# Kernel tuning notes

Measured on AMD Instinct MI355X. Metric: run time of the kernel, lower is better.

Reference implementation:

```python
import jax, jax.numpy as jnp
import numpy as np
from jax import lax

B, S, LQ, LS, D, F, FS, K, V = 32, 32, 30, 40, 300, 256, 3, 5, 100000


def setup_inputs() -> dict:
    key = jax.random.key(0)
    ks = jax.random.split(key, 8)
    return {
        "question": jax.random.randint(ks[0], (B, LQ), 0, V),
        "sentences": jax.random.randint(ks[1], (B, S, LS), 0, V),
        "target_sents": jax.random.randint(ks[2], (B, S), 0, 2),
        "target_docs": jax.random.randint(ks[3], (B,), 0, 2),
        "similarity_one_hot": (jax.random.uniform(ks[4], (B, S, LQ, LS)) < 0.05).astype(jnp.float32),
        "embeds": jax.random.normal(ks[5], (V, D), jnp.float32) * 0.1,
        "filters": jax.random.normal(ks[6], (F, FS, D), jnp.float32) * 0.1,
        "lin_w": jax.random.normal(ks[7], (6,), jnp.float32) * 0.3,
        "lin_b": jnp.zeros((), jnp.float32),
    }


def _conv_seq(x, W):
    # x: [..., L, D]; W: [F, fs, D]. Mirrors F.conv2d with padding=(fs//2+1, 0)
    # followed by keeping the LAST L output rows.
    fs = W.shape[1]
    pad = fs // 2 + 1
    L = x.shape[-2]
    lead = x.shape[:-2]
    xf = x.reshape((-1, L, x.shape[-1])).transpose(0, 2, 1)          # [N, D, L]
    out = lax.conv_general_dilated(
        xf, W.transpose(0, 2, 1), (1,), [(pad, pad)],
        dimension_numbers=("NCH", "OIH", "NCH"))                      # [N, F, L+2]
    out = out[:, :, -L:].transpose(0, 2, 1)                           # [N, L, F]
    return out.reshape(lead + (L, W.shape[0]))


def _cosine(Q, Sx):
    # Q: [B, LQ, d]; Sx: [B, S, LS, d] -> [B, S, LQ, LS]
    num = jnp.einsum("bqd,bsld->bsql", Q, Sx)
    qn = jnp.sqrt(jnp.sum(Q * Q, axis=-1))        # [B, LQ]
    sn = jnp.sqrt(jnp.sum(Sx * Sx, axis=-1))      # [B, S, LS]
    return num / (qn[:, None, :, None] * sn[:, :, None, :])


def _pool(sim):
    # sort + take top-k over last axis == top_k; features = (max, mean-of-top-k)
    vals = lax.top_k(sim, K)[0]                   # [..., K], descending
    return jnp.stack([vals[..., 0], vals.mean(-1)], axis=-1)  # [..., 2]


def _bce(p, t):
    logp = jnp.clip(jnp.log(p), -100.0)
    log1p = jnp.clip(jnp.log(1.0 - p), -100.0)
    return -(t * logp + (1.0 - t) * log1p).mean()


def reference(question, sentences, target_sents, target_docs, similarity_one_hot,
              embeds, filters, lin_w, lin_b):
    qe = embeds[question]                          # [B, LQ, D]
    se = embeds[sentences]                         # [B, S, LS, D]
    qc = _conv_seq(qe, filters)                    # [B, LQ, F]
    sc = _conv_seq(se, filters)                    # [B, S, LS, F]

    sim_ins = _cosine(qe, se)                      # [B, S, LQ, LS]
    sim_sen = _cosine(qc, sc)                      # [B, S, LQ, LS]

    feats = jnp.concatenate(
        [_pool(sim_ins), _pool(sim_sen), _pool(similarity_one_hot)], axis=-1)  # [B,S,LQ,6]
    lo = jax.nn.sigmoid(jnp.einsum("bsqf,f->bsq", feats, lin_w) + lin_b)        # [B,S,LQ]
    sent_output = lo.mean(-1)                      # [B, S]

    sent_loss = _bce_per_doc_mean(sent_output, target_sents.astype(jnp.float32))
    doc_em = sent_output.max(-1)                   # [B]
    doc_loss = _bce(doc_em, target_docs.astype(jnp.float32))
    total_loss = (sent_loss + doc_loss) / 2.0
    return (total_loss, sent_output, doc_em)


def _bce_per_doc_mean(p, t):
    # mean over docs of per-doc BCE (each a mean over sentences); equals global mean
    logp = jnp.clip(jnp.log(p), -100.0)
    log1p = jnp.clip(jnp.log(1.0 - p), -100.0)
    return -(t * logp + (1.0 - t) * log1p).mean(-1).mean()
```

## Files before the change

kernel.cpp:

```cpp
#include <hip/hip_runtime.h>
#include <math.h>


typedef __attribute__((ext_vector_type(4))) float f32x4;
typedef __attribute__((ext_vector_type(8))) short s16x8;

__device__ inline ushort bf16rne(float f) {
  unsigned u = __float_as_uint(f);
  u += 0x7fff + ((u >> 16) & 1);
  return (ushort)(u >> 16);
}
__device__ inline uint pack2(float a, float b) {
  return (uint)bf16rne(a) | ((uint)bf16rne(b) << 16);
}
__device__ inline float ubf(short h) { return __uint_as_float(((uint)(ushort)h) << 16); }

__global__ __launch_bounds__(64) void k_prepB(const float* __restrict__ filters,
                                              ushort* __restrict__ fB) {
  const int bid = blockIdx.x;
  const int lane = threadIdx.x;
  const int nt = bid & 15;
  const int tk = bid >> 4;
  const int tap = tk / 10, kstep = tk - tap * 10;
  const int f = nt * 16 + (lane & 15);
  const int kb = kstep * 32 + (lane >> 4) * 8;
  uint p[4];
#pragma unroll
  for (int h = 0; h < 4; ++h) {
    int d0 = kb + h * 2, d1 = kb + h * 2 + 1;
    float v0 = (d0 < 300) ? filters[(size_t)f * 900 + tap * 300 + d0] : 0.f;
    float v1 = (d1 < 300) ? filters[(size_t)f * 900 + tap * 300 + d1] : 0.f;
    p[h] = (uint)bf16rne(v0) | ((uint)bf16rne(v1) << 16);
  }
  uint4* dst = (uint4*)(fB + ((size_t)bid * 64 + lane) * 8);
  *dst = make_uint4(p[0], p[1], p[2], p[3]);
}

template<int L, int MT, int ROWS_ST>
__global__ __launch_bounds__(256) void k_conv_mfma(const int* __restrict__ tokens,
                                                   const float* __restrict__ embeds,
                                                   const ushort* __restrict__ fB,
                                                   ushort* __restrict__ blobA,
                                                   ushort* __restrict__ blobC,
                                                   float* __restrict__ rcpA,
                                                   float* __restrict__ rcpC) {
  constexpr int R320 = ROWS_ST * 320;
  __shared__ __align__(16) ushort xs[R320];
  __shared__ int tok[64];
  const int tid = threadIdx.x;
  const int seq = blockIdx.x;

  if (tid < L) tok[tid] = tokens[(size_t)seq * L + tid];
  __syncthreads();

  for (int idx = tid; idx < ROWS_ST * 80; idx += 256) {
    int row = idx / 80;
    int s = idx - row * 80;
    int d = s * 4;
    float4 v = make_float4(0.f, 0.f, 0.f, 0.f);
    if (row < L && d < 300) v = *(const float4*)(embeds + (size_t)tok[row] * 300 + d);
    int flat = row * 320 + d;
    int swz = flat ^ ((row & 7) << 3);
    *(uint2*)(xs + swz) = make_uint2(pack2(v.x, v.y), pack2(v.z, v.w));
  }
  __syncthreads();

  const int wv = tid >> 6, lane = tid & 63;
  const int lr = lane & 15, lh = lane >> 4;

  for (int t = wv; t < 10 * MT; t += 4) {
    int kstep = t / MT, tile = t - kstep * MT;
    int row = tile * 16 + lr;
    int flat = row * 320 + kstep * 32 + lh * 8;
    s16x8 v = *(const s16x8*)(xs + (flat ^ ((row & 7) << 3)));
    *(s16x8*)(blobA + ((((size_t)seq * 10 + kstep) * MT + tile) * 64 + lane) * 8) = v;
  }
  if (tid < L) {
    int row = tid;
    float s = 0.f;
    for (int c = 0; c < 40; ++c) {
      int flat = row * 320 + c * 8;
      s16x8 v = *(const s16x8*)(xs + (flat ^ ((row & 7) << 3)));
#pragma unroll
      for (int i = 0; i < 8; ++i) { float f = ubf(v[i]); s += f * f; }
    }
    rcpA[(size_t)seq * L + row] = (s > 0.f) ? rsqrtf(s) : 0.f;
  }

  f32x4 acc[MT][4];
#pragma unroll
  for (int mt = 0; mt < MT; ++mt)
#pragma unroll
    for (int n = 0; n < 4; ++n)
#pragma unroll
      for (int r = 0; r < 4; ++r) acc[mt][n][r] = 0.f;

  const s16x8* fBv = (const s16x8*)fB;
  for (int kstep = 0; kstep < 10; ++kstep) {
#pragma unroll
    for (int tap = 0; tap < 3; ++tap) {
      s16x8 b[4];
#pragma unroll
      for (int n = 0; n < 4; ++n)
        b[n] = fBv[((size_t)((tap * 10 + kstep) * 16 + (wv * 4 + n))) * 64 + lane];
#pragma unroll
      for (int mt = 0; mt < MT; ++mt) {
        int row = mt * 16 + lr + tap;
        int flat = row * 320 + kstep * 32 + lh * 8;
        s16x8 a = *(const s16x8*)(xs + (flat ^ ((row & 7) << 3)));
#pragma unroll
        for (int n = 0; n < 4; ++n)
          acc[mt][n] = __builtin_amdgcn_mfma_f32_16x16x32_bf16(a, b[n], acc[mt][n], 0, 0, 0);
      }
    }
  }
  __syncthreads();

#pragma unroll
  for (int mt = 0; mt < MT; ++mt)
#pragma unroll
    for (int n = 0; n < 4; ++n)
#pragma unroll
      for (int r = 0; r < 4; ++r) {
        int j = mt * 16 + lh * 4 + r;
        if (j < L) {
          int f = wv * 64 + n * 16 + lr;
          int flat = j * 320 + f;
          xs[flat ^ ((j & 7) << 3)] = bf16rne(acc[mt][n][r]);
        }
      }
  __syncthreads();

  for (int t = wv; t < 8 * MT; t += 4) {
    int kstep = t / MT, tile = t - kstep * MT;
    int row = tile * 16 + lr;
    int flat = row * 320 + kstep * 32 + lh * 8;
    s16x8 v = *(const s16x8*)(xs + (flat ^ ((row & 7) << 3)));
    *(s16x8*)(blobC + ((((size_t)seq * 8 + kstep) * MT + tile) * 64 + lane) * 8) = v;
  }
  if (tid < L) {
    int row = tid;
    float s = 0.f;
    for (int c = 0; c < 32; ++c) {
      int flat = row * 320 + c * 8;
      s16x8 v = *(const s16x8*)(xs + (flat ^ ((row & 7) << 3)));
#pragma unroll
      for (int i = 0; i < 8; ++i) { float f = ubf(v[i]); s += f * f; }
    }
    rcpC[(size_t)seq * L + row] = (s > 0.f) ? rsqrtf(s) : 0.f;
  }
}

__global__ __launch_bounds__(256, 6) void k_sim(const float* __restrict__ oneh,
                                                const ushort* __restrict__ qeb,
                                                const ushort* __restrict__ seb,
                                                const ushort* __restrict__ qcb,
                                                const ushort* __restrict__ scb,
                                                const float* __restrict__ rq0,
                                                const float* __restrict__ rs0,
                                                const float* __restrict__ rq1,
                                                const float* __restrict__ rs1,
                                                const float* __restrict__ lin_w,
                                                const float* __restrict__ lin_b,
                                                float* __restrict__ out) {
  const int bs = blockIdx.x;
  const int b = bs >> 5;
  const int tid = threadIdx.x;
  const int wv = tid >> 6, lane = tid & 63;
  const int lr = lane & 15, lh = lane >> 4;

  __shared__ float simb[2][30][49];
  __shared__ float ohl[30 * 41];
  __shared__ float rQ[2][30], rS[2][40];
  __shared__ float feats[30][6];
  __shared__ float lo[30];

  if (tid < 30) rQ[0][tid] = rq0[b * 30 + tid];
  else if (tid < 60) rQ[1][tid - 30] = rq1[b * 30 + (tid - 30)];
  else if (tid < 100) rS[0][tid - 60] = rs0[(size_t)bs * 40 + (tid - 60)];
  else if (tid < 140) rS[1][tid - 100] = rs1[(size_t)bs * 40 + (tid - 100)];
  {
    const float* og = oneh + (size_t)bs * 1200;
    for (int i = tid; i < 1200; i += 256) {
      int q = i / 40, l = i - q * 40;
      ohl[q * 41 + l] = og[i];
    }
  }
  __syncthreads();

  for (int task = wv; task < 6; task += 4) {
    int ph = task / 3, nt = task - ph * 3;
    int KS = ph ? 8 : 10;
    const ushort* Ab = ph ? (qcb + (size_t)b * 8 * 2 * 512) : (qeb + (size_t)b * 10 * 2 * 512);
    const ushort* Bb = ph ? (scb + (size_t)bs * 8 * 3 * 512) : (seb + (size_t)bs * 10 * 3 * 512);
    f32x4 acc0 = {0.f, 0.f, 0.f, 0.f};
    f32x4 acc1 = {0.f, 0.f, 0.f, 0.f};
    for (int k = 0; k < KS; ++k) {
      s16x8 bf = *(const s16x8*)(Bb + ((size_t)(k * 3 + nt) * 64 + lane) * 8);
      s16x8 a0 = *(const s16x8*)(Ab + ((size_t)(k * 2 + 0) * 64 + lane) * 8);
      s16x8 a1 = *(const s16x8*)(Ab + ((size_t)(k * 2 + 1) * 64 + lane) * 8);
      acc0 = __builtin_amdgcn_mfma_f32_16x16x32_bf16(a0, bf, acc0, 0, 0, 0);
      acc1 = __builtin_amdgcn_mfma_f32_16x16x32_bf16(a1, bf, acc1, 0, 0, 0);
    }
    int l = nt * 16 + lr;
    if (l < 40) {
#pragma unroll
      for (int r = 0; r < 4; ++r) {
        int q0 = lh * 4 + r;
        simb[ph][q0][l] = acc0[r] * rQ[ph][q0] * rS[ph][l];
        int q1 = 16 + lh * 4 + r;
        if (q1 < 30) simb[ph][q1][l] = acc1[r] * rQ[ph][q1] * rS[ph][l];
      }
    }
  }
  __syncthreads();

  if (tid < 90) {
    const int m = tid / 30, q = tid - m * 30;
    const float* row = (m == 0) ? &simb[0][q][0] : (m == 1) ? &simb[1][q][0] : (ohl + q * 41);
    float thr = 3.4e38f;
    int got = 0;
    float sum = 0.f, maxv = 0.f;
    while (got < 5) {
      float mx = -3.4e38f;
      int c = 0;
      for (int l = 0; l < 40; ++l) {
        float v = row[l];
        if (v < thr) {
          if (v > mx) { mx = v; c = 1; }
          else if (v == mx) { c++; }
        }
      }
      if (c == 0) break;
      if (got == 0) maxv = mx;
      int take = (c < 5 - got) ? c : (5 - got);
      sum += mx * (float)take;
      got += take;
      thr = mx;
    }
    feats[q][m * 2 + 0] = maxv;
    feats[q][m * 2 + 1] = sum * 0.2f;
  }
  __syncthreads();
  if (tid < 30) {
    float z = lin_b[0];
#pragma unroll
    for (int i = 0; i < 6; ++i) z += feats[tid][i] * lin_w[i];
    lo[tid] = 1.0f / (1.0f + expf(-z));
  }
  __syncthreads();
  if (tid == 0) {
    float sum = 0.f;
    for (int q = 0; q < 30; ++q) sum += lo[q];
    out[1 + bs] = sum * (1.0f / 30.0f);
  }
}

__global__ __launch_bounds__(256) void k_loss(const int* __restrict__ tsent,
                                              const int* __restrict__ tdoc,
                                              float* __restrict__ out) {
  __shared__ float red[256];
  __shared__ float sent_loss_sh;
  const int tid = threadIdx.x;
  float local = 0.f;
  for (int i = tid; i < 1024; i += 256) {
    float p = out[1 + i];
    float t = (float)tsent[i];
    float lp = fmaxf(logf(p), -100.f);
    float l1 = fmaxf(logf(1.f - p), -100.f);
    local += -(t * lp + (1.f - t) * l1);
  }
  red[tid] = local;
  __syncthreads();
  for (int off = 128; off > 0; off >>= 1) {
    if (tid < off) red[tid] += red[tid + off];
    __syncthreads();
  }
  if (tid == 0) sent_loss_sh = red[0] * (1.0f / 1024.0f);
  __syncthreads();
  float dterm = 0.f;
  if (tid < 32) {
    float mx = out[1 + tid * 32];
    for (int s2 = 1; s2 < 32; ++s2) mx = fmaxf(mx, out[1 + tid * 32 + s2]);
    out[1025 + tid] = mx;
    float t = (float)tdoc[tid];
    float lp = fmaxf(logf(mx), -100.f);
    float l1 = fmaxf(logf(1.f - mx), -100.f);
    dterm = -(t * lp + (1.f - t) * l1);
  }
  red[tid] = dterm;
  __syncthreads();
  for (int off = 128; off > 0; off >>= 1) {
    if (tid < off) red[tid] += red[tid + off];
    __syncthreads();
  }
  if (tid == 0) out[0] = 0.5f * (sent_loss_sh + red[0] * (1.0f / 32.0f));
}

extern "C" void kernel_launch(void* const* d_in, const int* in_sizes, int n_in,
                              void* d_out, int out_size, void* d_ws, size_t ws_size,
                              hipStream_t stream) {
  const int*   question     = (const int*)d_in[0];
  const int*   sentences    = (const int*)d_in[1];
  const int*   target_sents = (const int*)d_in[2];
  const int*   target_docs  = (const int*)d_in[3];
  const float* oneh         = (const float*)d_in[4];
  const float* embeds       = (const float*)d_in[5];
  const float* filters      = (const float*)d_in[6];
  const float* lin_w        = (const float*)d_in[7];
  const float* lin_b        = (const float*)d_in[8];
  float* out = (float*)d_out;

  ushort* fB  = (ushort*)d_ws;
  ushort* seb = fB  + 245760;
  ushort* scb = seb + 15728640;
  ushort* qeb = scb + 12582912;
  ushort* qcb = qeb + 327680;
  float*  rs0 = (float*)(qcb + 262144);
  float*  rs1 = rs0 + 40960;
  float*  rq0 = rs1 + 40960;
  float*  rq1 = rq0 + 960;

  k_prepB<<<480, 64, 0, stream>>>(filters, fB);
  k_conv_mfma<40, 3, 50><<<1024, 256, 0, stream>>>(sentences, embeds, fB, seb, scb, rs0, rs1);
  k_conv_mfma<30, 2, 34><<<32, 256, 0, stream>>>(question, embeds, fB, qeb, qcb, rq0, rq1);
  k_sim<<<1024, 256, 0, stream>>>(oneh, qeb, seb, qcb, scb, rq0, rs0, rq1, rs1,
                                  lin_w, lin_b, out);
  k_loss<<<1, 256, 0, stream>>>(target_sents, target_docs, out);
}
```

Before: 98.62 us.

## Fuse sentence conv into similarity kernel to avoid global intermediates

```diff
diff --git a/kernel.cpp b/kernel.cpp
--- a/kernel.cpp
+++ b/kernel.cpp
@@ -151,34 +151,36 @@
   }
 }
 
-__global__ __launch_bounds__(256, 6) void k_sim(const float* __restrict__ oneh,
-                                                const ushort* __restrict__ qeb,
-                                                const ushort* __restrict__ seb,
-                                                const ushort* __restrict__ qcb,
-                                                const ushort* __restrict__ scb,
-                                                const float* __restrict__ rq0,
-                                                const float* __restrict__ rs0,
-                                                const float* __restrict__ rq1,
-                                                const float* __restrict__ rs1,
-                                                const float* __restrict__ lin_w,
-                                                const float* __restrict__ lin_b,
-                                                float* __restrict__ out) {
+__global__ __launch_bounds__(256) void k_fused(const int* __restrict__ sentences,
+                                               const float* __restrict__ embeds,
+                                               const ushort* __restrict__ fB,
+                                               const ushort* __restrict__ qeb,
+                                               const ushort* __restrict__ qcb,
+                                               const float* __restrict__ rq0,
+                                               const float* __restrict__ rq1,
+                                               const float* __restrict__ oneh,
+                                               const float* __restrict__ lin_w,
+                                               const float* __restrict__ lin_b,
+                                               float* __restrict__ out) {
+  constexpr int L = 40, MT = 3, ROWS_ST = 50;
+  constexpr int R320 = ROWS_ST * 320;
+  __shared__ __align__(16) ushort xs[R320];
+  __shared__ int tok[48];
+  __shared__ float simb[2][30][49];
+  __shared__ float ohl[30 * 41];
+  __shared__ float rQ[2][30], rS[2][40];
+  __shared__ float feats[30][6];
+  __shared__ float lo[30];
+
   const int bs = blockIdx.x;
   const int b = bs >> 5;
   const int tid = threadIdx.x;
   const int wv = tid >> 6, lane = tid & 63;
   const int lr = lane & 15, lh = lane >> 4;
 
-  __shared__ float simb[2][30][49];
-  __shared__ float ohl[30 * 41];
-  __shared__ float rQ[2][30], rS[2][40];
-  __shared__ float feats[30][6];
-  __shared__ float lo[30];
-
-  if (tid < 30) rQ[0][tid] = rq0[b * 30 + tid];
-  else if (tid < 60) rQ[1][tid - 30] = rq1[b * 30 + (tid - 30)];
-  else if (tid < 100) rS[0][tid - 60] = rs0[(size_t)bs * 40 + (tid - 60)];
-  else if (tid < 140) rS[1][tid - 100] = rs1[(size_t)bs * 40 + (tid - 100)];
+  if (tid < 40) tok[tid] = sentences[(size_t)bs * 40 + tid];
+  else if (tid >= 64 && tid < 94) rQ[0][tid - 64] = rq0[b * 30 + (tid - 64)];
+  else if (tid >= 96 && tid < 126) rQ[1][tid - 96] = rq1[b * 30 + (tid - 96)];
   {
     const float* og = oneh + (size_t)bs * 1200;
     for (int i = tid; i < 1200; i += 256) {
@@ -188,28 +190,130 @@
   }
   __syncthreads();
 
-  for (int task = wv; task < 6; task += 4) {
-    int ph = task / 3, nt = task - ph * 3;
-    int KS = ph ? 8 : 10;
-    const ushort* Ab = ph ? (qcb + (size_t)b * 8 * 2 * 512) : (qeb + (size_t)b * 10 * 2 * 512);
-    const ushort* Bb = ph ? (scb + (size_t)bs * 8 * 3 * 512) : (seb + (size_t)bs * 10 * 3 * 512);
-    f32x4 acc0 = {0.f, 0.f, 0.f, 0.f};
-    f32x4 acc1 = {0.f, 0.f, 0.f, 0.f};
-    for (int k = 0; k < KS; ++k) {
-      s16x8 bf = *(const s16x8*)(Bb + ((size_t)(k * 3 + nt) * 64 + lane) * 8);
+  for (int idx = tid; idx < ROWS_ST * 80; idx += 256) {
+    int row = idx / 80;
+    int s = idx - row * 80;
+    int d = s * 4;
+    float4 v = make_float4(0.f, 0.f, 0.f, 0.f);
+    if (row < L && d < 300) v = *(const float4*)(embeds + (size_t)tok[row] * 300 + d);
+    int flat = row * 320 + d;
+    int swz = flat ^ ((row & 7) << 3);
+    *(uint2*)(xs + swz) = make_uint2(pack2(v.x, v.y), pack2(v.z, v.w));
+  }
+  __syncthreads();
+
+  f32x4 s0a = {0.f, 0.f, 0.f, 0.f}, s0b = {0.f, 0.f, 0.f, 0.f};
+  if (wv < 3) {
+    const ushort* Ab = qeb + (size_t)b * 10 * 2 * 512;
+    for (int k = 0; k < 10; ++k) {
+      int brow = wv * 16 + lr;
+      int bflat = brow * 320 + k * 32 + lh * 8;
+      s16x8 bf = *(const s16x8*)(xs + (bflat ^ ((brow & 7) << 3)));
       s16x8 a0 = *(const s16x8*)(Ab + ((size_t)(k * 2 + 0) * 64 + lane) * 8);
       s16x8 a1 = *(const s16x8*)(Ab + ((size_t)(k * 2 + 1) * 64 + lane) * 8);
-      acc0 = __builtin_amdgcn_mfma_f32_16x16x32_bf16(a0, bf, acc0, 0, 0, 0);
-      acc1 = __builtin_amdgcn_mfma_f32_16x16x32_bf16(a1, bf, acc1, 0, 0, 0);
-    }
-    int l = nt * 16 + lr;
+      s0a = __builtin_amdgcn_mfma_f32_16x16x32_bf16(a0, bf, s0a, 0, 0, 0);
+      s0b = __builtin_amdgcn_mfma_f32_16x16x32_bf16(a1, bf, s0b, 0, 0, 0);
+    }
+  } else if (lane < 40) {
+    float s = 0.f;
+    for (int c = 0; c < 40; ++c) {
+      int flat = lane * 320 + c * 8;
+      s16x8 v = *(const s16x8*)(xs + (flat ^ ((lane & 7) << 3)));
+#pragma unroll
+      for (int i = 0; i < 8; ++i) { float f = ubf(v[i]); s += f * f; }
+    }
+    rS[0][lane] = (s > 0.f) ? rsqrtf(s) : 0.f;
+  }
+  __syncthreads();
+  if (wv < 3) {
+    int l = wv * 16 + lr;
     if (l < 40) {
 #pragma unroll
       for (int r = 0; r < 4; ++r) {
         int q0 = lh * 4 + r;
-        simb[ph][q0][l] = acc0[r] * rQ[ph][q0] * rS[ph][l];
+        simb[0][q0][l] = s0a[r] * rQ[0][q0] * rS[0][l];
         int q1 = 16 + lh * 4 + r;
-        if (q1 < 30) simb[ph][q1][l] = acc1[r] * rQ[ph][q1] * rS[ph][l];
+        if (q1 < 30) simb[0][q1][l] = s0b[r] * rQ[0][q1] * rS[0][l];
+      }
+    }
+  }
+
+  f32x4 acc[MT][4];
+#pragma unroll
+  for (int mt = 0; mt < MT; ++mt)
+#pragma unroll
+    for (int n = 0; n < 4; ++n)
+#pragma unroll
+      for (int r = 0; r < 4; ++r) acc[mt][n][r] = 0.f;
+
+  const s16x8* fBv = (const s16x8*)fB;
+  for (int kstep = 0; kstep < 10; ++kstep) {
+#pragma unroll
+    for (int tap = 0; tap < 3; ++tap) {
+      s16x8 bb[4];
+#pragma unroll
+      for (int n = 0; n < 4; ++n)
+        bb[n] = fBv[((size_t)((tap * 10 + kstep) * 16 + (wv * 4 + n))) * 64 + lane];
+#pragma unroll
+      for (int mt = 0; mt < MT; ++mt) {
+        int row = mt * 16 + lr + tap;
+        int flat = row * 320 + kstep * 32 + lh * 8;
+        s16x8 a = *(const s16x8*)(xs + (flat ^ ((row & 7) << 3)));
+#pragma unroll
+        for (int n = 0; n < 4; ++n)
+          acc[mt][n] = __builtin_amdgcn_mfma_f32_16x16x32_bf16(a, bb[n], acc[mt][n], 0, 0, 0);
+      }
+    }
+  }
+  __syncthreads();
+
+#pragma unroll
+  for (int mt = 0; mt < MT; ++mt)
+#pragma unroll
+    for (int n = 0; n < 4; ++n)
+#pragma unroll
+      for (int r = 0; r < 4; ++r) {
+        int j = mt * 16 + lh * 4 + r;
+        if (j < L) {
+          int f = wv * 64 + n * 16 + lr;
+          int flat = j * 320 + f;
+          xs[flat ^ ((j & 7) << 3)] = bf16rne(acc[mt][n][r]);
+        }
+      }
+  __syncthreads();
+
+  f32x4 s1a = {0.f, 0.f, 0.f, 0.f}, s1b = {0.f, 0.f, 0.f, 0.f};
+  if (wv < 3) {
+    const ushort* Ab = qcb + (size_t)b * 8 * 2 * 512;
+    for (int k = 0; k < 8; ++k) {
+      int brow = wv * 16 + lr;
+      int bflat = brow * 320 + k * 32 + lh * 8;
+      s16x8 bf = *(const s16x8*)(xs + (bflat ^ ((brow & 7) << 3)));
+      s16x8 a0 = *(const s16x8*)(Ab + ((size_t)(k * 2 + 0) * 64 + lane) * 8);
+      s16x8 a1 = *(const s16x8*)(Ab + ((size_t)(k * 2 + 1) * 64 + lane) * 8);
+      s1a = __builtin_amdgcn_mfma_f32_16x16x32_bf16(a0, bf, s1a, 0, 0, 0);
+      s1b = __builtin_amdgcn_mfma_f32_16x16x32_bf16(a1, bf, s1b, 0, 0, 0);
+    }
+  } else if (lane < 40) {
+    float s = 0.f;
+    for (int c = 0; c < 32; ++c) {
+      int flat = lane * 320 + c * 8;
+      s16x8 v = *(const s16x8*)(xs + (flat ^ ((lane & 7) << 3)));
+#pragma unroll
+      for (int i = 0; i < 8; ++i) { float f = ubf(v[i]); s += f * f; }
+    }
+    rS[1][lane] = (s > 0.f) ? rsqrtf(s) : 0.f;
+  }
+  __syncthreads();
+  if (wv < 3) {
+    int l = wv * 16 + lr;
+    if (l < 40) {
+#pragma unroll
+      for (int r = 0; r < 4; ++r) {
+        int q0 = lh * 4 + r;
+        simb[1][q0][l] = s1a[r] * rQ[1][q0] * rS[1][l];
+        int q1 = 16 + lh * 4 + r;
+        if (q1 < 30) simb[1][q1][l] = s1b[r] * rQ[1][q1] * rS[1][l];
       }
     }
   }
@@ -312,19 +416,14 @@
   float* out = (float*)d_out;
 
   ushort* fB  = (ushort*)d_ws;
-  ushort* seb = fB  + 245760;
-  ushort* scb = seb + 15728640;
-  ushort* qeb = scb + 12582912;
+  ushort* qeb = fB  + 245760;
   ushort* qcb = qeb + 327680;
-  float*  rs0 = (float*)(qcb + 262144);
-  float*  rs1 = rs0 + 40960;
-  float*  rq0 = rs1 + 40960;
+  float*  rq0 = (float*)(qcb + 262144);
   float*  rq1 = rq0 + 960;
 
   k_prepB<<<480, 64, 0, stream>>>(filters, fB);
-  k_conv_mfma<40, 3, 50><<<1024, 256, 0, stream>>>(sentences, embeds, fB, seb, scb, rs0, rs1);
   k_conv_mfma<30, 2, 34><<<32, 256, 0, stream>>>(question, embeds, fB, qeb, qcb, rq0, rq1);
-  k_sim<<<1024, 256, 0, stream>>>(oneh, qeb, seb, qcb, scb, rq0, rs0, rq1, rs1,
-                                  lin_w, lin_b, out);
+  k_fused<<<1024, 256, 0, stream>>>(sentences, embeds, fB, qeb, qcb, rq0, rq1,
+                                    oneh, lin_w, lin_b, out);
   k_loss<<<1, 256, 0, stream>>>(target_sents, target_docs, out);
 }
```

Measured after the change: 112.9 us. 1.15x slower.

## Split embedding gather into prep kernel, merge conv launches, read sentence embeds from LDS in sim

Applied to the files above, without the earlier changes.

```diff
diff --git a/kernel.cpp b/kernel.cpp
--- a/kernel.cpp
+++ b/kernel.cpp
@@ -15,65 +15,84 @@
 }
 __device__ inline float ubf(short h) { return __uint_as_float(((uint)(ushort)h) << 16); }
 
-__global__ __launch_bounds__(64) void k_prepB(const float* __restrict__ filters,
-                                              ushort* __restrict__ fB) {
-  const int bid = blockIdx.x;
-  const int lane = threadIdx.x;
-  const int nt = bid & 15;
-  const int tk = bid >> 4;
-  const int tap = tk / 10, kstep = tk - tap * 10;
-  const int f = nt * 16 + (lane & 15);
-  const int kb = kstep * 32 + (lane >> 4) * 8;
-  uint p[4];
-#pragma unroll
-  for (int h = 0; h < 4; ++h) {
-    int d0 = kb + h * 2, d1 = kb + h * 2 + 1;
-    float v0 = (d0 < 300) ? filters[(size_t)f * 900 + tap * 300 + d0] : 0.f;
-    float v1 = (d1 < 300) ? filters[(size_t)f * 900 + tap * 300 + d1] : 0.f;
-    p[h] = (uint)bf16rne(v0) | ((uint)bf16rne(v1) << 16);
-  }
-  uint4* dst = (uint4*)(fB + ((size_t)bid * 64 + lane) * 8);
-  *dst = make_uint4(p[0], p[1], p[2], p[3]);
-}
-
-template<int L, int MT, int ROWS_ST>
-__global__ __launch_bounds__(256) void k_conv_mfma(const int* __restrict__ tokens,
-                                                   const float* __restrict__ embeds,
-                                                   const ushort* __restrict__ fB,
-                                                   ushort* __restrict__ blobA,
-                                                   ushort* __restrict__ blobC,
-                                                   float* __restrict__ rcpA,
-                                                   float* __restrict__ rcpC) {
-  constexpr int R320 = ROWS_ST * 320;
-  __shared__ __align__(16) ushort xs[R320];
+__global__ __launch_bounds__(256) void k_prep_gather(const float* __restrict__ filters,
+                                                     ushort* __restrict__ fB,
+                                                     const int* __restrict__ question,
+                                                     const int* __restrict__ sentences,
+                                                     const float* __restrict__ embeds,
+                                                     ushort* __restrict__ xsg) {
   __shared__ int tok[64];
+  const int blk = blockIdx.x;
   const int tid = threadIdx.x;
-  const int seq = blockIdx.x;
-
-  if (tid < L) tok[tid] = tokens[(size_t)seq * L + tid];
-  __syncthreads();
-
-  for (int idx = tid; idx < ROWS_ST * 80; idx += 256) {
-    int row = idx / 80;
-    int s = idx - row * 80;
-    int d = s * 4;
-    float4 v = make_float4(0.f, 0.f, 0.f, 0.f);
-    if (row < L && d < 300) v = *(const float4*)(embeds + (size_t)tok[row] * 300 + d);
-    int flat = row * 320 + d;
-    int swz = flat ^ ((row & 7) << 3);
-    *(uint2*)(xs + swz) = make_uint2(pack2(v.x, v.y), pack2(v.z, v.w));
+  if (blk < 120) {
+    const int bid = blk * 4 + (tid >> 6);
+    const int lane = tid & 63;
+    const int nt = bid & 15;
+    const int tk = bid >> 4;
+    const int tap = tk / 10, kstep = tk - tap * 10;
+    const int f = nt * 16 + (lane & 15);
+    const int kb = kstep * 32 + (lane >> 4) * 8;
+    uint p[4];
+#pragma unroll
+    for (int h = 0; h < 4; ++h) {
+      int d0 = kb + h * 2, d1 = kb + h * 2 + 1;
+      float v0 = (d0 < 300) ? filters[(size_t)f * 900 + tap * 300 + d0] : 0.f;
+      float v1 = (d1 < 300) ? filters[(size_t)f * 900 + tap * 300 + d1] : 0.f;
+      p[h] = (uint)bf16rne(v0) | ((uint)bf16rne(v1) << 16);
+    }
+    *(uint4*)(fB + ((size_t)bid * 64 + lane) * 8) = make_uint4(p[0], p[1], p[2], p[3]);
+  } else {
+    const int g = blk - 120;
+    const int L = (g < 1024) ? 40 : 30;
+    const int ROWS = (g < 1024) ? 50 : 34;
+    const int* tokens = (g < 1024) ? (sentences + (size_t)g * 40)
+                                   : (question + (size_t)(g - 1024) * 30);
+    if (tid < L) tok[tid] = tokens[tid];
+    __syncthreads();
+    ushort* dst = xsg + (size_t)g * 16000;
+    const int items = ROWS * 80;
+    for (int idx = tid; idx < items; idx += 256) {
+      int row = idx / 80;
+      int d = (idx - row * 80) * 4;
+      float4 v = make_float4(0.f, 0.f, 0.f, 0.f);
+      if (row < L && d < 300) v = *(const float4*)(embeds + (size_t)tok[row] * 300 + d);
+      int flat = row * 320 + d;
+      *(uint2*)(dst + (flat ^ ((row & 7) << 3))) =
+          make_uint2(pack2(v.x, v.y), pack2(v.z, v.w));
+    }
+  }
+}
+
+template<int L, int MT, int ROWS_ST, bool EMIT_A>
+__device__ __forceinline__ void conv_body(int slot, int seq,
+                                          const ushort* __restrict__ xsg,
+                                          const ushort* __restrict__ fB,
+                                          ushort* __restrict__ blobA,
+                                          ushort* __restrict__ blobC,
+                                          float* __restrict__ rcpA,
+                                          float* __restrict__ rcpC,
+                                          ushort* xs) {
+  const int tid = threadIdx.x;
+
+  {
+    const uint4* src = (const uint4*)(xsg + (size_t)slot * 16000);
+    uint4* dst = (uint4*)xs;
+    constexpr int NV = ROWS_ST * 40;
+    for (int i = tid; i < NV; i += 256) dst[i] = src[i];
   }
   __syncthreads();
 
   const int wv = tid >> 6, lane = tid & 63;
   const int lr = lane & 15, lh = lane >> 4;
 
-  for (int t = wv; t < 10 * MT; t += 4) {
-    int kstep = t / MT, tile = t - kstep * MT;
-    int row = tile * 16 + lr;
-    int flat = row * 320 + kstep * 32 + lh * 8;
-    s16x8 v = *(const s16x8*)(xs + (flat ^ ((row & 7) << 3)));
-    *(s16x8*)(blobA + ((((size_t)seq * 10 + kstep) * MT + tile) * 64 + lane) * 8) = v;
+  if (EMIT_A) {
+    for (int t = wv; t < 10 * MT; t += 4) {
+      int kstep = t / MT, tile = t - kstep * MT;
+      int row = tile * 16 + lr;
+      int flat = row * 320 + kstep * 32 + lh * 8;
+      s16x8 v = *(const s16x8*)(xs + (flat ^ ((row & 7) << 3)));
+      *(s16x8*)(blobA + ((((size_t)seq * 10 + kstep) * MT + tile) * 64 + lane) * 8) = v;
+    }
   }
   if (tid < L) {
     int row = tid;
@@ -151,24 +170,43 @@
   }
 }
 
-__global__ __launch_bounds__(256, 6) void k_sim(const float* __restrict__ oneh,
-                                                const ushort* __restrict__ qeb,
-                                                const ushort* __restrict__ seb,
-                                                const ushort* __restrict__ qcb,
-                                                const ushort* __restrict__ scb,
-                                                const float* __restrict__ rq0,
-                                                const float* __restrict__ rs0,
-                                                const float* __restrict__ rq1,
-                                                const float* __restrict__ rs1,
-                                                const float* __restrict__ lin_w,
-                                                const float* __restrict__ lin_b,
-                                                float* __restrict__ out) {
+__global__ __launch_bounds__(256) void k_conv_all(const ushort* __restrict__ xsg,
+                                                  const ushort* __restrict__ fB,
+                                                  ushort* __restrict__ scb,
+                                                  ushort* __restrict__ qeb,
+                                                  ushort* __restrict__ qcb,
+                                                  float* __restrict__ rs0,
+                                                  float* __restrict__ rs1,
+                                                  float* __restrict__ rq0,
+                                                  float* __restrict__ rq1) {
+  __shared__ __align__(16) ushort xs[50 * 320];
+  const int bid = blockIdx.x;
+  if (bid < 1024) {
+    conv_body<40, 3, 50, false>(bid, bid, xsg, fB, nullptr, scb, rs0, rs1, xs);
+  } else {
+    conv_body<30, 2, 34, true>(bid, bid - 1024, xsg, fB, qeb, qcb, rq0, rq1, xs);
+  }
+}
+
+__global__ __launch_bounds__(256) void k_sim(const float* __restrict__ oneh,
+                                             const ushort* __restrict__ xsg,
+                                             const ushort* __restrict__ qeb,
+                                             const ushort* __restrict__ qcb,
+                                             const ushort* __restrict__ scb,
+                                             const float* __restrict__ rq0,
+                                             const float* __restrict__ rs0,
+                                             const float* __restrict__ rq1,
+                                             const float* __restrict__ rs1,
+                                             const float* __restrict__ lin_w,
+                                             const float* __restrict__ lin_b,
+                                             float* __restrict__ out) {
   const int bs = blockIdx.x;
   const int b = bs >> 5;
   const int tid = threadIdx.x;
   const int wv = tid >> 6, lane = tid & 63;
   const int lr = lane & 15, lh = lane >> 4;
 
+  __shared__ __align__(16) ushort xs2[48 * 320];
   __shared__ float simb[2][30][49];
   __shared__ float ohl[30 * 41];
   __shared__ float rQ[2][30], rS[2][40];
@@ -186,17 +224,29 @@
       ohl[q * 41 + l] = og[i];
     }
   }
+  {
+    const uint4* src = (const uint4*)(xsg + (size_t)bs * 16000);
+    uint4* dst = (uint4*)xs2;
+    for (int i = tid; i < 1920; i += 256) dst[i] = src[i];
+  }
   __syncthreads();
 
   for (int task = wv; task < 6; task += 4) {
     int ph = task / 3, nt = task - ph * 3;
     int KS = ph ? 8 : 10;
     const ushort* Ab = ph ? (qcb + (size_t)b * 8 * 2 * 512) : (qeb + (size_t)b * 10 * 2 * 512);
-    const ushort* Bb = ph ? (scb + (size_t)bs * 8 * 3 * 512) : (seb + (size_t)bs * 10 * 3 * 512);
+    const ushort* Bb = scb + (size_t)bs * 8 * 3 * 512;
     f32x4 acc0 = {0.f, 0.f, 0.f, 0.f};
     f32x4 acc1 = {0.f, 0.f, 0.f, 0.f};
+    int brow = nt * 16 + lr;
     for (int k = 0; k < KS; ++k) {
-      s16x8 bf = *(const s16x8*)(Bb + ((size_t)(k * 3 + nt) * 64 + lane) * 8);
+      s16x8 bf;
+      if (ph == 0) {
+        int flat = brow * 320 + k * 32 + lh * 8;
+        bf = *(const s16x8*)(xs2 + (flat ^ ((brow & 7) << 3)));
+      } else {
+        bf = *(const s16x8*)(Bb + ((size_t)(k * 3 + nt) * 64 + lane) * 8);
+      }
       s16x8 a0 = *(const s16x8*)(Ab + ((size_t)(k * 2 + 0) * 64 + lane) * 8);
       s16x8 a1 = *(const s16x8*)(Ab + ((size_t)(k * 2 + 1) * 64 + lane) * 8);
       acc0 = __builtin_amdgcn_mfma_f32_16x16x32_bf16(a0, bf, acc0, 0, 0, 0);
@@ -312,8 +362,8 @@
   float* out = (float*)d_out;
 
   ushort* fB  = (ushort*)d_ws;
-  ushort* seb = fB  + 245760;
-  ushort* scb = seb + 15728640;
+  ushort* xsg = fB  + 245760;
+  ushort* scb = xsg + 16896000;
   ushort* qeb = scb + 12582912;
   ushort* qcb = qeb + 327680;
   float*  rs0 = (float*)(qcb + 262144);
@@ -321,10 +371,9 @@
   float*  rq0 = rs1 + 40960;
   float*  rq1 = rq0 + 960;
 
-  k_prepB<<<480, 64, 0, stream>>>(filters, fB);
-  k_conv_mfma<40, 3, 50><<<1024, 256, 0, stream>>>(sentences, embeds, fB, seb, scb, rs0, rs1);
-  k_conv_mfma<30, 2, 34><<<32, 256, 0, stream>>>(question, embeds, fB, qeb, qcb, rq0, rq1);
-  k_sim<<<1024, 256, 0, stream>>>(oneh, qeb, seb, qcb, scb, rq0, rs0, rq1, rs1,
+  k_prep_gather<<<1176, 256, 0, stream>>>(filters, fB, question, sentences, embeds, xsg);
+  k_conv_all<<<1056, 256, 0, stream>>>(xsg, fB, scb, qeb, qcb, rs0, rs1, rq0, rq1);
+  k_sim<<<1024, 256, 0, stream>>>(oneh, xsg, qeb, qcb, scb, rq0, rs0, rq1, rs1,
                                   lin_w, lin_b, out);
   k_loss<<<1, 256, 0, stream>>>(target_sents, target_docs, out);
 }
```

Result: slower. 124.7 us (+26.5%).
